# Kernel tuning notes

Measured on AMD Instinct MI355X. Metric: run time of the kernel, lower is better.

The kernel has to match this reference:

```python
import jax, jax.numpy as jnp
import numpy as np

TAU = 0.8
LAMBDA_BALANCE = 0.05
EPS = 1e-8


def setup_inputs() -> dict:
    key = jax.random.key(0)
    ks = jax.random.split(key, 8)
    B, Din, Dh, Dout, E = 8192, 1024, 2048, 1024, 8
    x = jax.random.normal(ks[0], (B, Din), jnp.float32)
    # gumbel noise for F.gumbel_softmax: g = -log(-log(U)), U~Uniform(0,1)
    u = jax.random.uniform(ks[1], (B, E), jnp.float32, 1e-6, 1.0 - 1e-6)
    gumbel = -jnp.log(-jnp.log(u))
    gate_w = jax.random.normal(ks[2], (Din, E), jnp.float32) * 0.02
    gate_b = jnp.zeros((E,), jnp.float32)
    w1 = jax.random.normal(ks[3], (E, Din, Dh), jnp.float32) * (1.0 / np.sqrt(Din))
    b1 = jnp.zeros((E, Dh), jnp.float32)
    w2 = jax.random.normal(ks[4], (E, Dh, Dout), jnp.float32) * (1.0 / np.sqrt(Dh))
    b2 = jnp.zeros((E, Dout), jnp.float32)
    return dict(x=x, gumbel=gumbel, gate_w=gate_w, gate_b=gate_b,
                w1=w1, b1=b1, w2=w2, b2=b2)


def reference(x, gumbel, gate_w, gate_b, w1, b1, w2, b2):
    # gating logits [B, E]
    logits = x @ gate_w + gate_b
    # gumbel-softmax (soft), tau=0.8 -> selection probs (selection_policy='soft')
    probs = jax.nn.softmax((logits + gumbel) / TAU, axis=1)
    # load-balancing auxiliary loss
    router_probs = jax.nn.softmax(logits / TAU, axis=1)
    importance = router_probs.mean(axis=0)  # [E]
    load = probs.mean(axis=0)               # [E]
    importance_cv = jnp.std(importance, ddof=1) / (importance.mean() + EPS)
    load_cv = jnp.std(load, ddof=1) / (load.mean() + EPS)
    E = probs.shape[1]
    switch_loss = E * jnp.sum(importance * load)
    aux_loss = (switch_loss + importance_cv + load_cv) * LAMBDA_BALANCE
    # dense all-expert MLP stack: h [E,B,Dh], eo [E,B,Dout]
    h = jax.nn.relu(jnp.einsum('bd,edh->ebh', x, w1) + b1[:, None, :])
    eo = jnp.einsum('ebh,eho->ebo', h, w2) + b2[:, None, :]
    # bmm combine: expert_outputs [B, Dout, E] @ probs [B, E, 1] -> [B, Dout]
    output = jnp.einsum('ebo,be->bo', eo, probs)
    return output, aux_loss
```

## Files before the change

### kernel.cpp

```cpp
#include <hip/hip_runtime.h>

typedef __attribute__((ext_vector_type(4))) float f4;
typedef __attribute__((ext_vector_type(8))) short s8;

__device__ inline float b2f(unsigned int u) {
    unsigned int v = u << 16;
    float f;
    __builtin_memcpy(&f, &v, 4);
    return f;
}
__device__ inline unsigned short f2b(float f) {
    unsigned int u;
    __builtin_memcpy(&u, &f, 4);
    unsigned int r = u + 0x7fffu + ((u >> 16) & 1u);
    return (unsigned short)(r >> 16);
}
__device__ inline void async16(const void* g, void* l) {
    __builtin_amdgcn_global_load_lds(
        (const __attribute__((address_space(1))) unsigned int*)g,
        (__attribute__((address_space(3))) unsigned int*)l, 16, 0, 0);
}

#define B_ROWS 8192
#define DIN 1024
#define DH 2048
#define DOUT 1024
#define NE 8
#define NCAT 16384

__global__ __launch_bounds__(64) void detect_dtype(const unsigned short* __restrict__ p, int* __restrict__ flag)
{
    const int lane = threadIdx.x;
    int sane = 0;
    for (int i = lane; i < 4096; i += 64) {
        const float a = fabsf(b2f(p[i]));
        if (a > 1e-30f && a < 1e3f) sane++;
    }
    for (int off = 32; off; off >>= 1) sane += __shfl_xor(sane, off, 64);
    if (lane == 0) *flag = (sane < 3600) ? 1 : 0;
}

__global__ __launch_bounds__(256) void normalize_kernel(const void* __restrict__ src,
                                                        unsigned short* __restrict__ dst,
                                                        const int* __restrict__ flag, int n)
{
    const int i = blockIdx.x * 256 + threadIdx.x;
    if (i >= n) return;
    if (*flag) dst[i] = f2b(((const float*)src)[i]);
    else       dst[i] = ((const unsigned short*)src)[i];
}

__global__ __launch_bounds__(256) void gating_kernel(
    const unsigned short* __restrict__ x, const unsigned short* __restrict__ gum,
    const unsigned short* __restrict__ gw, const unsigned short* __restrict__ gb,
    float* __restrict__ probs, float* __restrict__ partials)
{
    const int t = threadIdx.x, wave = t >> 6, lane = t & 63;
    float sp = 0.f, sr = 0.f;
    const int base = blockIdx.x * 32 + wave * 8;
    for (int rr = 0; rr < 8; rr++) {
        const int b = base + rr;
        float acc[8];
#pragma unroll
        for (int e = 0; e < 8; e++) acc[e] = 0.f;
        for (int kk = 0; kk < 16; kk++) {
            const int k = kk * 64 + lane;
            const float xv = b2f(x[(size_t)b * DIN + k]);
            const uint4 wv = *(const uint4*)(gw + (size_t)k * 8);
            acc[0] += xv * b2f(wv.x & 0xffffu); acc[1] += xv * b2f(wv.x >> 16);
            acc[2] += xv * b2f(wv.y & 0xffffu); acc[3] += xv * b2f(wv.y >> 16);
            acc[4] += xv * b2f(wv.z & 0xffffu); acc[5] += xv * b2f(wv.z >> 16);
            acc[6] += xv * b2f(wv.w & 0xffffu); acc[7] += xv * b2f(wv.w >> 16);
        }
#pragma unroll
        for (int e = 0; e < 8; e++)
            for (int off = 32; off; off >>= 1) acc[e] += __shfl_xor(acc[e], off, 64);
        float lg[8], p1[8], p2[8];
        float m1 = -1e30f, m2 = -1e30f;
#pragma unroll
        for (int e = 0; e < 8; e++) {
            lg[e] = acc[e] + b2f(gb[e]);
            p1[e] = (lg[e] + b2f(gum[(size_t)b * 8 + e])) * 1.25f;
            p2[e] = lg[e] * 1.25f;
            m1 = fmaxf(m1, p1[e]); m2 = fmaxf(m2, p2[e]);
        }
        float s1 = 0.f, s2 = 0.f;
#pragma unroll
        for (int e = 0; e < 8; e++) {
            p1[e] = expf(p1[e] - m1); s1 += p1[e];
            p2[e] = expf(p2[e] - m2); s2 += p2[e];
        }
        const float i1 = 1.f / s1, i2 = 1.f / s2;
        if (lane < 8) {
            const float pv = p1[lane] * i1;
            probs[(size_t)b * 8 + lane] = pv;
            sp += pv;
            sr += p2[lane] * i2;
        }
    }
    __shared__ float red[4][16];
    if (lane < 8) { red[wave][lane] = sp; red[wave][8 + lane] = sr; }
    __syncthreads();
    if (t < 16)
        partials[blockIdx.x * 16 + t] = red[0][t] + red[1][t] + red[2][t] + red[3][t];
}

__global__ void aux_finalize(const float* __restrict__ partials, void* __restrict__ outp,
                             const int* __restrict__ flag)
{
    __shared__ float fin[16];
    const int t = threadIdx.x;
    if (t < 16) {
        float s = 0.f;
        for (int i = 0; i < 256; i++) s += partials[i * 16 + t];
        fin[t] = s;
    }
    __syncthreads();
    if (t == 0) {
        float ld[8], im[8];
        for (int e = 0; e < 8; e++) { ld[e] = fin[e] / 8192.f; im[e] = fin[8 + e] / 8192.f; }
        float mi = 0.f, ml = 0.f;
        for (int e = 0; e < 8; e++) { mi += im[e]; ml += ld[e]; }
        mi *= 0.125f; ml *= 0.125f;
        float vi = 0.f, vl = 0.f, sw = 0.f;
        for (int e = 0; e < 8; e++) {
            vi += (im[e] - mi) * (im[e] - mi);
            vl += (ld[e] - ml) * (ld[e] - ml);
            sw += im[e] * ld[e];
        }
        const float cvi = sqrtf(vi / 7.f) / (mi + 1e-8f);
        const float cvl = sqrtf(vl / 7.f) / (ml + 1e-8f);
        const float aux = (8.f * sw + cvi + cvl) * 0.05f;
        if (*flag) ((float*)outp)[8388608] = aux;
        else       ((unsigned short*)outp)[8388608] = f2b(aux);
    }
}

__global__ __launch_bounds__(256) void transpose_cvt(
    const void* __restrict__ src, unsigned short* __restrict__ out,
    int R, int C, int ldOut, size_t outEStride, const int* __restrict__ flag)
{
    __shared__ unsigned short tile[64][65];
    const int e = blockIdx.z;
    const size_t eoff = (size_t)e * R * C;
    unsigned short* op = out + (size_t)e * outEStride;
    const int fl = *flag;
    const int tx = threadIdx.x, ty = threadIdx.y;
    const int r0 = blockIdx.y * 64, c0 = blockIdx.x * 64;
    if (fl) {
        const float* in = (const float*)src + eoff;
#pragma unroll
        for (int i = 0; i < 16; i++) {
            const int r = ty + i * 4;
            tile[r][tx] = f2b(in[(size_t)(r0 + r) * C + c0 + tx]);
        }
    } else {
        const unsigned short* in = (const unsigned short*)src + eoff;
#pragma unroll
        for (int i = 0; i < 16; i++) {
            const int r = ty + i * 4;
            tile[r][tx] = in[(size_t)(r0 + r) * C + c0 + tx];
        }
    }
    __syncthreads();
#pragma unroll
    for (int i = 0; i < 16; i++) {
        const int c = ty + i * 4;
        op[(size_t)(c0 + c) * ldOut + r0 + tx] = tile[tx][c];
    }
}

#define MFMA16(a, b, c) __builtin_amdgcn_mfma_f32_16x16x32_bf16(a, b, c, 0, 0, 0)

template<int K, int EPI>
__global__ __launch_bounds__(512, 2) void gemm256(
    const unsigned short* __restrict__ A,
    const unsigned short* __restrict__ Bt,
    const unsigned short* __restrict__ bias,
    const float* __restrict__ probs,
    unsigned short* __restrict__ outH,
    float* __restrict__ partial,
    int rows, int klen, int SWZ)
{
    __shared__ __align__(16) char smem[131072];
    const int t = threadIdx.x;
    const int w = t >> 6, l = t & 63;
    const int l15 = l & 15, q = l >> 4;
    const int wm = w >> 2, wn = w & 3;

    int bx = blockIdx.x, by = blockIdx.y;
    if (SWZ) {
        const int n = gridDim.x * gridDim.y;
        int bid = by * gridDim.x + bx;
        const int c = n >> 3;
        bid = (bid & 7) * c + (bid >> 3);
        bx = bid % gridDim.x; by = bid / gridDim.x;
    }
    const int m0 = bx * 256, n0 = by * 256;
    const int kstart = blockIdx.z * klen;
    const int NT = klen >> 6;

    const int srow = l >> 3;
    const int swz = (l & 7) ^ srow;
    const char* pa[4]; const char* pb[4];
#pragma unroll
    for (int i = 0; i < 4; i++) {
        const int ra = m0 + (w * 4 + i) * 8 + srow;
        const int rb = n0 + (w * 4 + i) * 8 + srow;
        pa[i] = (const char*)(A  + (size_t)ra * K + kstart + swz * 8);
        pb[i] = (const char*)(Bt + (size_t)rb * K + kstart + swz * 8);
    }

    auto stage = [&](int kt, int bsel) {
        char* Ab = smem + bsel * 65536;
        char* Bb = Ab + 32768;
        const size_t kb = (size_t)kt * 128;
#pragma unroll
        for (int i = 0; i < 4; i++) async16(pa[i] + kb, Ab + (w * 4 + i) * 1024);
#pragma unroll
        for (int i = 0; i < 4; i++) async16(pb[i] + kb, Bb + (w * 4 + i) * 1024);
    };

    f4 acc[8][4];
#pragma unroll
    for (int i = 0; i < 8; i++)
#pragma unroll
        for (int j = 0; j < 4; j++) { acc[i][j][0] = 0.f; acc[i][j][1] = 0.f; acc[i][j][2] = 0.f; acc[i][j][3] = 0.f; }

    const int arow0 = (wm * 128 + l15) * 128;
    const int brow0 = (wn * 64 + l15) * 128;
    int sz[2];
#pragma unroll
    for (int kh = 0; kh < 2; kh++) sz[kh] = (((kh * 4 + q) ^ (l & 7)) << 4);

    stage(0, 0);
    stage(1, 1);

    for (int kt = 0; kt < NT; ++kt) {
        if (kt + 1 < NT) asm volatile("s_waitcnt vmcnt(8)" ::: "memory");
        else             asm volatile("s_waitcnt vmcnt(0)" ::: "memory");
        __builtin_amdgcn_s_barrier();
        const char* Ab = smem + (kt & 1) * 65536;
        const char* Bb = Ab + 32768;
        s8 Af[4][2], Bf[4][2];
#pragma unroll
        for (int mf = 0; mf < 4; mf++)
#pragma unroll
            for (int kh = 0; kh < 2; kh++)
                Af[mf][kh] = *(const s8*)(Ab + arow0 + mf * 2048 + sz[kh]);
#pragma unroll
        for (int nf = 0; nf < 4; nf++)
#pragma unroll
            for (int kh = 0; kh < 2; kh++)
                Bf[nf][kh] = *(const s8*)(Bb + brow0 + nf * 2048 + sz[kh]);
        __builtin_amdgcn_s_setprio(1);
#pragma unroll
        for (int mf = 0; mf < 4; mf++)
#pragma unroll
            for (int nf = 0; nf < 4; nf++) {
                acc[mf][nf] = MFMA16(Af[mf][0], Bf[nf][0], acc[mf][nf]);
                acc[mf][nf] = MFMA16(Af[mf][1], Bf[nf][1], acc[mf][nf]);
            }
        __builtin_amdgcn_s_setprio(0);
#pragma unroll
        for (int mf = 0; mf < 4; mf++)
#pragma unroll
            for (int kh = 0; kh < 2; kh++)
                Af[mf][kh] = *(const s8*)(Ab + arow0 + (mf + 4) * 2048 + sz[kh]);
        __builtin_amdgcn_s_setprio(1);
#pragma unroll
        for (int mf = 0; mf < 4; mf++)
#pragma unroll
            for (int nf = 0; nf < 4; nf++) {
                acc[mf + 4][nf] = MFMA16(Af[mf][0], Bf[nf][0], acc[mf + 4][nf]);
                acc[mf + 4][nf] = MFMA16(Af[mf][1], Bf[nf][1], acc[mf + 4][nf]);
            }
        __builtin_amdgcn_s_setprio(0);
        asm volatile("s_waitcnt lgkmcnt(0)" ::: "memory");
        __builtin_amdgcn_sched_barrier(0);
        __builtin_amdgcn_s_barrier();
        if (kt + 2 < NT) stage(kt + 2, kt & 1);
    }

    if (EPI == 0) {
#pragma unroll
        for (int nf = 0; nf < 4; nf++) {
            const int gn = n0 + wn * 64 + nf * 16 + l15;
            const int e = gn >> 11;
            const float bval = b2f(bias[gn]);
#pragma unroll
            for (int mf = 0; mf < 8; mf++) {
                const int gmB = m0 + wm * 128 + mf * 16 + q * 4;
#pragma unroll
                for (int r = 0; r < 4; r++) {
                    const int gm = gmB + r;
                    const float pv = probs[(size_t)gm * 8 + e];
                    const float v = fmaxf(acc[mf][nf][r] + bval, 0.f) * pv;
                    outH[(size_t)gm * NCAT + gn] = f2b(v);
                }
            }
        }
    } else {
        float* pp = partial + (size_t)blockIdx.z * rows * DOUT;
#pragma unroll
        for (int mf = 0; mf < 8; mf++) {
            const int gmB = m0 + wm * 128 + mf * 16 + q * 4;
#pragma unroll
            for (int nf = 0; nf < 4; nf++) {
                const int gn = n0 + wn * 64 + nf * 16 + l15;
#pragma unroll
                for (int r = 0; r < 4; r++)
                    pp[(size_t)(gmB + r) * DOUT + gn] = acc[mf][nf][r];
            }
        }
    }
}

__global__ __launch_bounds__(256) void out_finalize(
    const float* __restrict__ partial, const unsigned short* __restrict__ b2,
    const float* __restrict__ probs, void* __restrict__ outp, size_t outOff,
    const int* __restrict__ flag, int rows, int nks)
{
    const int idx = blockIdx.x * 256 + threadIdx.x;
    if (idx >= rows * DOUT) return;
    const int m = idx >> 10, n = idx & (DOUT - 1);
    float v = 0.f;
    for (int ks = 0; ks < nks; ks++)
        v += partial[(size_t)ks * rows * DOUT + idx];
    const f4 p0 = *(const f4*)(probs + (size_t)m * 8);
    const f4 p1 = *(const f4*)(probs + (size_t)m * 8 + 4);
    v += p0[0] * b2f(b2[n])            + p0[1] * b2f(b2[DOUT + n])
       + p0[2] * b2f(b2[2 * DOUT + n]) + p0[3] * b2f(b2[3 * DOUT + n])
       + p1[0] * b2f(b2[4 * DOUT + n]) + p1[1] * b2f(b2[5 * DOUT + n])
       + p1[2] * b2f(b2[6 * DOUT + n]) + p1[3] * b2f(b2[7 * DOUT + n]);
    const size_t oi = outOff + ((size_t)m * DOUT) + n;
    if (*flag) ((float*)outp)[oi] = v;
    else       ((unsigned short*)outp)[oi] = f2b(v);
}

extern "C" void kernel_launch(void* const* d_in, const int* in_sizes, int n_in,
                              void* d_out, int out_size, void* d_ws, size_t ws_size,
                              hipStream_t stream)
{
    const void* x   = d_in[0];
    const void* gum = d_in[1];
    const void* gw  = d_in[2];
    const void* gb  = d_in[3];
    const void* w1  = d_in[4];
    const void* b1  = d_in[5];
    const void* w2  = d_in[6];
    const void* b2  = d_in[7];

    char* ws = (char*)d_ws;
    size_t cur = 0;
    auto alloc = [&](size_t bytes) { size_t p = cur; cur = (cur + bytes + 255) & ~(size_t)255; return p; };

    int* flag              = (int*)(ws + alloc(256));
    float* probs           = (float*)(ws + alloc(8192 * 8 * 4));
    float* partials        = (float*)(ws + alloc(256 * 16 * 4));
    unsigned short* xn     = (unsigned short*)(ws + alloc((size_t)B_ROWS * DIN * 2));
    unsigned short* gumn   = (unsigned short*)(ws + alloc((size_t)B_ROWS * 8 * 2));
    unsigned short* gwn    = (unsigned short*)(ws + alloc((size_t)DIN * 8 * 2));
    unsigned short* gbn    = (unsigned short*)(ws + alloc(8 * 2));
    unsigned short* b1n    = (unsigned short*)(ws + alloc((size_t)NE * DH * 2));
    unsigned short* b2n    = (unsigned short*)(ws + alloc((size_t)NE * DOUT * 2));
    unsigned short* w1Tcat = (unsigned short*)(ws + alloc((size_t)NCAT * DIN * 2));
    unsigned short* w2Tcat = (unsigned short*)(ws + alloc((size_t)DOUT * NCAT * 2));
    const size_t fixed = cur;

    int R = B_ROWS, KS;
    for (;;) {
        KS = 16384 / R;
        const size_t need = fixed + (size_t)R * (NCAT * 2) + (size_t)KS * R * DOUT * 4;
        if (R <= 512 || need <= ws_size) break;
        R >>= 1;
    }
    const int klen = 16384 / KS;
    unsigned short* Hcat = (unsigned short*)(ws + fixed);
    float* partial = (float*)(ws + fixed + (size_t)R * (NCAT * 2));

    detect_dtype<<<1, 64, 0, stream>>>((const unsigned short*)x, flag);

    normalize_kernel<<<(B_ROWS * DIN + 255) / 256, 256, 0, stream>>>(x, xn, flag, B_ROWS * DIN);
    normalize_kernel<<<(B_ROWS * 8 + 255) / 256, 256, 0, stream>>>(gum, gumn, flag, B_ROWS * 8);
    normalize_kernel<<<(DIN * 8 + 255) / 256, 256, 0, stream>>>(gw, gwn, flag, DIN * 8);
    normalize_kernel<<<1, 256, 0, stream>>>(gb, gbn, flag, 8);
    normalize_kernel<<<(NE * DH + 255) / 256, 256, 0, stream>>>(b1, b1n, flag, NE * DH);
    normalize_kernel<<<(NE * DOUT + 255) / 256, 256, 0, stream>>>(b2, b2n, flag, NE * DOUT);

    gating_kernel<<<256, 256, 0, stream>>>(xn, gumn, gwn, gbn, probs, partials);
    aux_finalize<<<1, 64, 0, stream>>>(partials, d_out, flag);

    transpose_cvt<<<dim3(DH / 64, DIN / 64, NE), dim3(64, 4), 0, stream>>>(
        w1, w1Tcat, DIN, DH, DIN, (size_t)DH * DIN, flag);
    transpose_cvt<<<dim3(DOUT / 64, DH / 64, NE), dim3(64, 4), 0, stream>>>(
        w2, w2Tcat, DH, DOUT, NCAT, (size_t)DH, flag);

    for (int c0 = 0; c0 < B_ROWS; c0 += R) {
        gemm256<DIN, 0><<<dim3(R / 256, NCAT / 256, 1), 512, 0, stream>>>(
            xn + (size_t)c0 * DIN, w1Tcat, b1n, probs + (size_t)c0 * 8, Hcat,
            nullptr, R, DIN, 1);
        gemm256<NCAT, 1><<<dim3(R / 256, DOUT / 256, KS), 512, 0, stream>>>(
            Hcat, w2Tcat, nullptr, nullptr, nullptr,
            partial, R, klen, 0);
        out_finalize<<<(R * DOUT) / 256, 256, 0, stream>>>(
            partial, b2n, probs + (size_t)c0 * 8, d_out, (size_t)c0 * DOUT, flag, R, KS);
    }
}
```

Measured before the change: 1.057 ms.

## Restructure GEMM main loop into four interleaved load/MFMA phases per k-tile

Rewrites the GEMM k-loop so that each 64-wide k-tile is split into two k-halves with separate LDS sub-buffers. Each half is processed in two phases, and every phase issues a slice of the next tile's async global-to-LDS loads before its MFMAs. The shared-memory layout and XOR swizzle change to 64-byte rows per k-half, and the prefetch distance drops from two tiles to one. The goal is to spread load issue across the compute and cut stalls from bulk staging. The cost is more barriers per tile and less lookahead on global memory latency.

```diff
diff --git a/kernel.cpp b/kernel.cpp
--- a/kernel.cpp
+++ b/kernel.cpp
@@ -172,6 +172,46 @@
 
 #define MFMA16(a, b, c) __builtin_amdgcn_mfma_f32_16x16x32_bf16(a, b, c, 0, 0, 0)
 
+#define PHASE(KH, NFH, STAGE_STMT, TAIL_STMT)                                   \
+    {                                                                           \
+        if ((NFH) == 0) {                                                       \
+            _Pragma("unroll")                                                   \
+            for (int mf = 0; mf < 8; mf++)                                      \
+                Af[mf] = *(const s8*)(Ab + (KH) * 16384 + aoff[mf]);            \
+        }                                                                       \
+        const s8 Bf0 = *(const s8*)(Bb + (KH) * 16384 + boff[(NFH) * 2 + 0]);   \
+        const s8 Bf1 = *(const s8*)(Bb + (KH) * 16384 + boff[(NFH) * 2 + 1]);   \
+        STAGE_STMT;                                                             \
+        __builtin_amdgcn_s_barrier();                                           \
+        __builtin_amdgcn_s_setprio(1);                                          \
+        _Pragma("unroll")                                                       \
+        for (int mf = 0; mf < 8; mf++) {                                        \
+            acc[mf][(NFH) * 2 + 0] = MFMA16(Af[mf], Bf0, acc[mf][(NFH) * 2 + 0]); \
+            acc[mf][(NFH) * 2 + 1] = MFMA16(Af[mf], Bf1, acc[mf][(NFH) * 2 + 1]); \
+        }                                                                       \
+        __builtin_amdgcn_s_setprio(0);                                          \
+        TAIL_STMT;                                                              \
+        __builtin_amdgcn_s_barrier();                                           \
+    }
+
+#define STG_A(nd, kh, ktn)                                                      \
+    {                                                                           \
+        char* dst_ = smem + (nd) * 65536 + (kh) * 16384 + w2 * 1024;            \
+        const size_t kb_ = (size_t)(ktn) * 128 + (kh) * 64;                     \
+        async16(paC0 + kb_, dst_);                                              \
+        async16(paC1 + kb_, dst_ + 1024);                                       \
+    }
+#define STG_B(nd, kh, ktn)                                                      \
+    {                                                                           \
+        char* dst_ = smem + (nd) * 65536 + 32768 + (kh) * 16384 + w2 * 1024;    \
+        const size_t kb_ = (size_t)(ktn) * 128 + (kh) * 64;                     \
+        async16(pbC0 + kb_, dst_);                                              \
+        async16(pbC1 + kb_, dst_ + 1024);                                       \
+    }
+
+#define VM4  asm volatile("s_waitcnt vmcnt(4)" ::: "memory")
+#define VM0  asm volatile("s_waitcnt vmcnt(0)" ::: "memory")
+
 template<int K, int EPI>
 __global__ __launch_bounds__(512, 2) void gemm256(
     const unsigned short* __restrict__ A,
@@ -200,26 +240,21 @@
     const int kstart = blockIdx.z * klen;
     const int NT = klen >> 6;
 
-    const int srow = l >> 3;
-    const int swz = (l & 7) ^ srow;
-    const char* pa[4]; const char* pb[4];
-#pragma unroll
-    for (int i = 0; i < 4; i++) {
-        const int ra = m0 + (w * 4 + i) * 8 + srow;
-        const int rb = n0 + (w * 4 + i) * 8 + srow;
-        pa[i] = (const char*)(A  + (size_t)ra * K + kstart + swz * 8);
-        pb[i] = (const char*)(Bt + (size_t)rb * K + kstart + swz * 8);
-    }
-
-    auto stage = [&](int kt, int bsel) {
-        char* Ab = smem + bsel * 65536;
-        char* Bb = Ab + 32768;
-        const size_t kb = (size_t)kt * 128;
-#pragma unroll
-        for (int i = 0; i < 4; i++) async16(pa[i] + kb, Ab + (w * 4 + i) * 1024);
-#pragma unroll
-        for (int i = 0; i < 4; i++) async16(pb[i] + kb, Bb + (w * 4 + i) * 1024);
-    };
+    const int w2 = w * 2;
+    const int srow0 = w2 * 16 + (l >> 2);
+    const int srow1 = srow0 + 16;
+    const int gr = ((l & 3) ^ ((l >> 3) & 3)) * 8;
+    const char* paC0 = (const char*)(A  + (size_t)(m0 + srow0) * K + kstart + gr);
+    const char* paC1 = (const char*)(A  + (size_t)(m0 + srow1) * K + kstart + gr);
+    const char* pbC0 = (const char*)(Bt + (size_t)(n0 + srow0) * K + kstart + gr);
+    const char* pbC1 = (const char*)(Bt + (size_t)(n0 + srow1) * K + kstart + gr);
+
+    const int skey = ((q ^ ((l15 >> 1) & 3)) << 4);
+    int aoff[8]; int boff[4];
+#pragma unroll
+    for (int mf = 0; mf < 8; mf++) aoff[mf] = (wm * 128 + mf * 16 + l15) * 64 + skey;
+#pragma unroll
+    for (int nf = 0; nf < 4; nf++) boff[nf] = (wn * 64 + nf * 16 + l15) * 64 + skey;
 
     f4 acc[8][4];
 #pragma unroll
@@ -227,59 +262,30 @@
 #pragma unroll
         for (int j = 0; j < 4; j++) { acc[i][j][0] = 0.f; acc[i][j][1] = 0.f; acc[i][j][2] = 0.f; acc[i][j][3] = 0.f; }
 
-    const int arow0 = (wm * 128 + l15) * 128;
-    const int brow0 = (wn * 64 + l15) * 128;
-    int sz[2];
-#pragma unroll
-    for (int kh = 0; kh < 2; kh++) sz[kh] = (((kh * 4 + q) ^ (l & 7)) << 4);
-
-    stage(0, 0);
-    stage(1, 1);
-
-    for (int kt = 0; kt < NT; ++kt) {
-        if (kt + 1 < NT) asm volatile("s_waitcnt vmcnt(8)" ::: "memory");
-        else             asm volatile("s_waitcnt vmcnt(0)" ::: "memory");
-        __builtin_amdgcn_s_barrier();
-        const char* Ab = smem + (kt & 1) * 65536;
+    s8 Af[8];
+
+    STG_A(0, 0, 0); STG_B(0, 0, 0); STG_A(0, 1, 0); STG_B(0, 1, 0);
+    VM4;
+    __builtin_amdgcn_s_barrier();
+
+    int kt = 0;
+    for (; kt + 1 < NT; ++kt) {
+        const int d = kt & 1, nd = d ^ 1;
+        const char* Ab = smem + d * 65536;
         const char* Bb = Ab + 32768;
-        s8 Af[4][2], Bf[4][2];
-#pragma unroll
-        for (int mf = 0; mf < 4; mf++)
-#pragma unroll
-            for (int kh = 0; kh < 2; kh++)
-                Af[mf][kh] = *(const s8*)(Ab + arow0 + mf * 2048 + sz[kh]);
-#pragma unroll
-        for (int nf = 0; nf < 4; nf++)
-#pragma unroll
-            for (int kh = 0; kh < 2; kh++)
-                Bf[nf][kh] = *(const s8*)(Bb + brow0 + nf * 2048 + sz[kh]);
-        __builtin_amdgcn_s_setprio(1);
-#pragma unroll
-        for (int mf = 0; mf < 4; mf++)
-#pragma unroll
-            for (int nf = 0; nf < 4; nf++) {
-                acc[mf][nf] = MFMA16(Af[mf][0], Bf[nf][0], acc[mf][nf]);
-                acc[mf][nf] = MFMA16(Af[mf][1], Bf[nf][1], acc[mf][nf]);
-            }
-        __builtin_amdgcn_s_setprio(0);
-#pragma unroll
-        for (int mf = 0; mf < 4; mf++)
-#pragma unroll
-            for (int kh = 0; kh < 2; kh++)
-                Af[mf][kh] = *(const s8*)(Ab + arow0 + (mf + 4) * 2048 + sz[kh]);
-        __builtin_amdgcn_s_setprio(1);
-#pragma unroll
-        for (int mf = 0; mf < 4; mf++)
-#pragma unroll
-            for (int nf = 0; nf < 4; nf++) {
-                acc[mf + 4][nf] = MFMA16(Af[mf][0], Bf[nf][0], acc[mf + 4][nf]);
-                acc[mf + 4][nf] = MFMA16(Af[mf][1], Bf[nf][1], acc[mf + 4][nf]);
-            }
-        __builtin_amdgcn_s_setprio(0);
-        asm volatile("s_waitcnt lgkmcnt(0)" ::: "memory");
-        __builtin_amdgcn_sched_barrier(0);
-        __builtin_amdgcn_s_barrier();
-        if (kt + 2 < NT) stage(kt + 2, kt & 1);
+        PHASE(0, 0, STG_A(nd, 0, kt + 1), (void)0)
+        PHASE(0, 1, STG_B(nd, 0, kt + 1), VM4)
+        PHASE(1, 0, STG_A(nd, 1, kt + 1), (void)0)
+        PHASE(1, 1, STG_B(nd, 1, kt + 1), VM4)
+    }
+    {
+        const int d = kt & 1;
+        const char* Ab = smem + d * 65536;
+        const char* Bb = Ab + 32768;
+        PHASE(0, 0, (void)0, (void)0)
+        PHASE(0, 1, (void)0, VM0)
+        PHASE(1, 0, (void)0, (void)0)
+        PHASE(1, 1, (void)0, (void)0)
     }
 
     if (EPI == 0) {
```

Measured after the change: 1.033 ms. 2.3% less time.

## Split GEMMs into specialized kernels with smaller K-tiles and row chunking

Applied to the files above, without the earlier changes.

Replaces the templated 256x256 GEMM, which used a 64-wide K tile and 128KB of LDS, with two specialized kernels. Both use 32-wide K tiles and simpler double buffering with __syncthreads, targeting higher occupancy (launch bounds 4). The second GEMM uses 256x128 tiles so more blocks can run. Rows are processed in chunks of 2048 rather than the full batch, which lowers the split-K factor and workspace needs. In exchange there are more barriers per unit of K, less reuse per tile in the second GEMM, and the explicit vmcnt waits and setprio scheduling are gone.

```diff
diff --git a/kernel.cpp b/kernel.cpp
--- a/kernel.cpp
+++ b/kernel.cpp
@@ -172,146 +172,171 @@
 
 #define MFMA16(a, b, c) __builtin_amdgcn_mfma_f32_16x16x32_bf16(a, b, c, 0, 0, 0)
 
-template<int K, int EPI>
-__global__ __launch_bounds__(512, 2) void gemm256(
+__global__ __launch_bounds__(512, 4) void gemm_h2(
     const unsigned short* __restrict__ A,
     const unsigned short* __restrict__ Bt,
     const unsigned short* __restrict__ bias,
     const float* __restrict__ probs,
-    unsigned short* __restrict__ outH,
-    float* __restrict__ partial,
-    int rows, int klen, int SWZ)
-{
-    __shared__ __align__(16) char smem[131072];
+    unsigned short* __restrict__ outH)
+{
+    constexpr int K = DIN;
+    __shared__ __align__(16) char smem[65536];
     const int t = threadIdx.x;
     const int w = t >> 6, l = t & 63;
     const int l15 = l & 15, q = l >> 4;
     const int wm = w >> 2, wn = w & 3;
 
-    int bx = blockIdx.x, by = blockIdx.y;
-    if (SWZ) {
-        const int n = gridDim.x * gridDim.y;
-        int bid = by * gridDim.x + bx;
-        const int c = n >> 3;
-        bid = (bid & 7) * c + (bid >> 3);
-        bx = bid % gridDim.x; by = bid / gridDim.x;
-    }
+    int bid = blockIdx.y * gridDim.x + blockIdx.x;
+    const int cpx = (gridDim.x * gridDim.y) >> 3;
+    bid = (bid & 7) * cpx + (bid >> 3);
+    const int bx = bid % gridDim.x, by = bid / gridDim.x;
     const int m0 = bx * 256, n0 = by * 256;
+
+    const int srow = l >> 2;
+    const int gr = ((l & 3) ^ ((l >> 3) & 3)) * 8;
+    const unsigned short* pa0 = A  + (size_t)(m0 + w * 32 + srow) * K + gr;
+    const unsigned short* pa1 = pa0 + (size_t)16 * K;
+    const unsigned short* pb0 = Bt + (size_t)(n0 + w * 32 + srow) * K + gr;
+    const unsigned short* pb1 = pb0 + (size_t)16 * K;
+
+    const int skey = ((q ^ ((l15 >> 1) & 3)) << 4);
+    int aoff[8], boff[4];
+#pragma unroll
+    for (int mf = 0; mf < 8; mf++) aoff[mf] = (wm * 128 + mf * 16 + l15) * 64 + skey;
+#pragma unroll
+    for (int nf = 0; nf < 4; nf++) boff[nf] = (wn * 64 + nf * 16 + l15) * 64 + skey;
+
+    f4 acc[8][4];
+#pragma unroll
+    for (int i = 0; i < 8; i++)
+#pragma unroll
+        for (int j = 0; j < 4; j++) { acc[i][j][0] = 0.f; acc[i][j][1] = 0.f; acc[i][j][2] = 0.f; acc[i][j][3] = 0.f; }
+
+    {
+        char* Ab = smem; char* Bb = smem + 16384;
+        async16(pa0, Ab + w * 2048); async16(pa1, Ab + w * 2048 + 1024);
+        async16(pb0, Bb + w * 2048); async16(pb1, Bb + w * 2048 + 1024);
+    }
+    __syncthreads();
+
+    int cur = 0;
+    for (int k0 = 0; k0 < K; k0 += 32) {
+        if (k0 + 32 < K) {
+            char* Ab = smem + (cur ^ 1) * 32768; char* Bb = Ab + 16384;
+            const int kn = k0 + 32;
+            async16(pa0 + kn, Ab + w * 2048); async16(pa1 + kn, Ab + w * 2048 + 1024);
+            async16(pb0 + kn, Bb + w * 2048); async16(pb1 + kn, Bb + w * 2048 + 1024);
+        }
+        const char* Ab = smem + cur * 32768;
+        const char* Bb = Ab + 16384;
+        s8 Af[8], Bf[4];
+#pragma unroll
+        for (int mf = 0; mf < 8; mf++) Af[mf] = *(const s8*)(Ab + aoff[mf]);
+#pragma unroll
+        for (int nf = 0; nf < 4; nf++) Bf[nf] = *(const s8*)(Bb + boff[nf]);
+#pragma unroll
+        for (int mf = 0; mf < 8; mf++)
+#pragma unroll
+            for (int nf = 0; nf < 4; nf++)
+                acc[mf][nf] = MFMA16(Af[mf], Bf[nf], acc[mf][nf]);
+        __syncthreads();
+        cur ^= 1;
+    }
+
+#pragma unroll
+    for (int nf = 0; nf < 4; nf++) {
+        const int gn = n0 + wn * 64 + nf * 16 + l15;
+        const int e = gn >> 11;
+        const float bval = b2f(bias[gn]);
+#pragma unroll
+        for (int mf = 0; mf < 8; mf++) {
+            const int gmB = m0 + wm * 128 + mf * 16 + q * 4;
+#pragma unroll
+            for (int r = 0; r < 4; r++) {
+                const int gm = gmB + r;
+                const float pv = probs[(size_t)gm * 8 + e];
+                const float v = fmaxf(acc[mf][nf][r] + bval, 0.f) * pv;
+                outH[(size_t)gm * NCAT + gn] = f2b(v);
+            }
+        }
+    }
+}
+
+__global__ __launch_bounds__(512, 4) void gemm_o2(
+    const unsigned short* __restrict__ A,
+    const unsigned short* __restrict__ Bt,
+    float* __restrict__ partial, int rows, int klen)
+{
+    constexpr int K = NCAT;
+    __shared__ __align__(16) char smem[49152];
+    const int t = threadIdx.x;
+    const int w = t >> 6, l = t & 63;
+    const int l15 = l & 15, q = l >> 4;
+    const int wm = w >> 1, wn = w & 1;
+
+    const int m0 = blockIdx.x * 256, n0 = blockIdx.y * 128;
     const int kstart = blockIdx.z * klen;
-    const int NT = klen >> 6;
-
-    const int srow = l >> 3;
-    const int swz = (l & 7) ^ srow;
-    const char* pa[4]; const char* pb[4];
-#pragma unroll
-    for (int i = 0; i < 4; i++) {
-        const int ra = m0 + (w * 4 + i) * 8 + srow;
-        const int rb = n0 + (w * 4 + i) * 8 + srow;
-        pa[i] = (const char*)(A  + (size_t)ra * K + kstart + swz * 8);
-        pb[i] = (const char*)(Bt + (size_t)rb * K + kstart + swz * 8);
-    }
-
-    auto stage = [&](int kt, int bsel) {
-        char* Ab = smem + bsel * 65536;
-        char* Bb = Ab + 32768;
-        const size_t kb = (size_t)kt * 128;
-#pragma unroll
-        for (int i = 0; i < 4; i++) async16(pa[i] + kb, Ab + (w * 4 + i) * 1024);
-#pragma unroll
-        for (int i = 0; i < 4; i++) async16(pb[i] + kb, Bb + (w * 4 + i) * 1024);
-    };
-
-    f4 acc[8][4];
-#pragma unroll
-    for (int i = 0; i < 8; i++)
+
+    const int srow = l >> 2;
+    const int gr = ((l & 3) ^ ((l >> 3) & 3)) * 8;
+    const unsigned short* pa0 = A  + (size_t)(m0 + w * 32 + srow) * K + kstart + gr;
+    const unsigned short* pa1 = pa0 + (size_t)16 * K;
+    const unsigned short* pb0 = Bt + (size_t)(n0 + w * 16 + srow) * K + kstart + gr;
+
+    const int skey = ((q ^ ((l15 >> 1) & 3)) << 4);
+    int aoff[4], boff[4];
+#pragma unroll
+    for (int mf = 0; mf < 4; mf++) aoff[mf] = (wm * 64 + mf * 16 + l15) * 64 + skey;
+#pragma unroll
+    for (int nf = 0; nf < 4; nf++) boff[nf] = (wn * 64 + nf * 16 + l15) * 64 + skey;
+
+    f4 acc[4][4];
+#pragma unroll
+    for (int i = 0; i < 4; i++)
 #pragma unroll
         for (int j = 0; j < 4; j++) { acc[i][j][0] = 0.f; acc[i][j][1] = 0.f; acc[i][j][2] = 0.f; acc[i][j][3] = 0.f; }
 
-    const int arow0 = (wm * 128 + l15) * 128;
-    const int brow0 = (wn * 64 + l15) * 128;
-    int sz[2];
-#pragma unroll
-    for (int kh = 0; kh < 2; kh++) sz[kh] = (((kh * 4 + q) ^ (l & 7)) << 4);
-
-    stage(0, 0);
-    stage(1, 1);
-
-    for (int kt = 0; kt < NT; ++kt) {
-        if (kt + 1 < NT) asm volatile("s_waitcnt vmcnt(8)" ::: "memory");
-        else             asm volatile("s_waitcnt vmcnt(0)" ::: "memory");
-        __builtin_amdgcn_s_barrier();
-        const char* Ab = smem + (kt & 1) * 65536;
-        const char* Bb = Ab + 32768;
-        s8 Af[4][2], Bf[4][2];
+    {
+        char* Ab = smem; char* Bb = smem + 16384;
+        async16(pa0, Ab + w * 2048); async16(pa1, Ab + w * 2048 + 1024);
+        async16(pb0, Bb + w * 1024);
+    }
+    __syncthreads();
+
+    int cur = 0;
+    for (int k0 = 0; k0 < klen; k0 += 32) {
+        if (k0 + 32 < klen) {
+            char* Ab = smem + (cur ^ 1) * 24576; char* Bb = Ab + 16384;
+            const int kn = k0 + 32;
+            async16(pa0 + kn, Ab + w * 2048); async16(pa1 + kn, Ab + w * 2048 + 1024);
+            async16(pb0 + kn, Bb + w * 1024);
+        }
+        const char* Ab = smem + cur * 24576;
+        const char* Bb = Ab + 16384;
+        s8 Af[4], Bf[4];
+#pragma unroll
+        for (int mf = 0; mf < 4; mf++) Af[mf] = *(const s8*)(Ab + aoff[mf]);
+#pragma unroll
+        for (int nf = 0; nf < 4; nf++) Bf[nf] = *(const s8*)(Bb + boff[nf]);
 #pragma unroll
         for (int mf = 0; mf < 4; mf++)
 #pragma unroll
-            for (int kh = 0; kh < 2; kh++)
-                Af[mf][kh] = *(const s8*)(Ab + arow0 + mf * 2048 + sz[kh]);
-#pragma unroll
-        for (int nf = 0; nf < 4; nf++)
-#pragma unroll
-            for (int kh = 0; kh < 2; kh++)
-                Bf[nf][kh] = *(const s8*)(Bb + brow0 + nf * 2048 + sz[kh]);
-        __builtin_amdgcn_s_setprio(1);
-#pragma unroll
-        for (int mf = 0; mf < 4; mf++)
-#pragma unroll
-            for (int nf = 0; nf < 4; nf++) {
-                acc[mf][nf] = MFMA16(Af[mf][0], Bf[nf][0], acc[mf][nf]);
-                acc[mf][nf] = MFMA16(Af[mf][1], Bf[nf][1], acc[mf][nf]);
-            }
-        __builtin_amdgcn_s_setprio(0);
-#pragma unroll
-        for (int mf = 0; mf < 4; mf++)
-#pragma unroll
-            for (int kh = 0; kh < 2; kh++)
-                Af[mf][kh] = *(const s8*)(Ab + arow0 + (mf + 4) * 2048 + sz[kh]);
-        __builtin_amdgcn_s_setprio(1);
-#pragma unroll
-        for (int mf = 0; mf < 4; mf++)
-#pragma unroll
-            for (int nf = 0; nf < 4; nf++) {
-                acc[mf + 4][nf] = MFMA16(Af[mf][0], Bf[nf][0], acc[mf + 4][nf]);
-                acc[mf + 4][nf] = MFMA16(Af[mf][1], Bf[nf][1], acc[mf + 4][nf]);
-            }
-        __builtin_amdgcn_s_setprio(0);
-        asm volatile("s_waitcnt lgkmcnt(0)" ::: "memory");
-        __builtin_amdgcn_sched_barrier(0);
-        __builtin_amdgcn_s_barrier();
-        if (kt + 2 < NT) stage(kt + 2, kt & 1);
-    }
-
-    if (EPI == 0) {
+            for (int nf = 0; nf < 4; nf++)
+                acc[mf][nf] = MFMA16(Af[mf], Bf[nf], acc[mf][nf]);
+        __syncthreads();
+        cur ^= 1;
+    }
+
+    float* pp = partial + (size_t)blockIdx.z * rows * DOUT;
+#pragma unroll
+    for (int mf = 0; mf < 4; mf++) {
+        const int gmB = m0 + wm * 64 + mf * 16 + q * 4;
 #pragma unroll
         for (int nf = 0; nf < 4; nf++) {
             const int gn = n0 + wn * 64 + nf * 16 + l15;
-            const int e = gn >> 11;
-            const float bval = b2f(bias[gn]);
-#pragma unroll
-            for (int mf = 0; mf < 8; mf++) {
-                const int gmB = m0 + wm * 128 + mf * 16 + q * 4;
-#pragma unroll
-                for (int r = 0; r < 4; r++) {
-                    const int gm = gmB + r;
-                    const float pv = probs[(size_t)gm * 8 + e];
-                    const float v = fmaxf(acc[mf][nf][r] + bval, 0.f) * pv;
-                    outH[(size_t)gm * NCAT + gn] = f2b(v);
-                }
-            }
-        }
-    } else {
-        float* pp = partial + (size_t)blockIdx.z * rows * DOUT;
-#pragma unroll
-        for (int mf = 0; mf < 8; mf++) {
-            const int gmB = m0 + wm * 128 + mf * 16 + q * 4;
-#pragma unroll
-            for (int nf = 0; nf < 4; nf++) {
-                const int gn = n0 + wn * 64 + nf * 16 + l15;
-#pragma unroll
-                for (int r = 0; r < 4; r++)
-                    pp[(size_t)(gmB + r) * DOUT + gn] = acc[mf][nf][r];
-            }
+#pragma unroll
+            for (int r = 0; r < 4; r++)
+                pp[(size_t)(gmB + r) * DOUT + gn] = acc[mf][nf][r];
         }
     }
 }
@@ -368,7 +393,7 @@
     unsigned short* w2Tcat = (unsigned short*)(ws + alloc((size_t)DOUT * NCAT * 2));
     const size_t fixed = cur;
 
-    int R = B_ROWS, KS;
+    int R = 2048, KS;
     for (;;) {
         KS = 16384 / R;
         const size_t need = fixed + (size_t)R * (NCAT * 2) + (size_t)KS * R * DOUT * 4;
@@ -397,12 +422,10 @@
         w2, w2Tcat, DH, DOUT, NCAT, (size_t)DH, flag);
 
     for (int c0 = 0; c0 < B_ROWS; c0 += R) {
-        gemm256<DIN, 0><<<dim3(R / 256, NCAT / 256, 1), 512, 0, stream>>>(
-            xn + (size_t)c0 * DIN, w1Tcat, b1n, probs + (size_t)c0 * 8, Hcat,
-            nullptr, R, DIN, 1);
-        gemm256<NCAT, 1><<<dim3(R / 256, DOUT / 256, KS), 512, 0, stream>>>(
-            Hcat, w2Tcat, nullptr, nullptr, nullptr,
-            partial, R, klen, 0);
+        gemm_h2<<<dim3(R / 256, NCAT / 256), 512, 0, stream>>>(
+            xn + (size_t)c0 * DIN, w1Tcat, b1n, probs + (size_t)c0 * 8, Hcat);
+        gemm_o2<<<dim3(R / 256, DOUT / 128, KS), 512, 0, stream>>>(
+            Hcat, w2Tcat, partial, R, klen);
         out_finalize<<<(R * DOUT) / 256, 256, 0, stream>>>(
             partial, b2n, probs + (size_t)c0 * 8, d_out, (size_t)c0 * DOUT, flag, R, KS);
     }
```

Result: slower. 2.422 ms (+129.2%).
